# Kernel tuning notes

Hardware: AMD Instinct MI355X
Metric: run time of the kernel (lower is better)

The kernel has to match this reference:

```python
import jax, jax.numpy as jnp
import numpy as np

N = 50000   # nodes
E = 800000  # edges (avg degree 16)
D = 96      # feature dim for all layers


def setup_inputs() -> dict:
    key = jax.random.key(0)
    ks = jax.random.split(key, 8)
    x = jax.random.normal(ks[0], (N, D), dtype=jnp.float32)
    edge_index = jax.random.randint(ks[1], (2, E), 0, N, dtype=jnp.int32)
    edge_weight = jax.random.uniform(ks[2], (E,), dtype=jnp.float32)
    batch = jnp.zeros((N,), dtype=jnp.int32)  # unused by forward, kept for signature fidelity
    s = 1.0 / np.sqrt(D)
    W1 = jax.random.normal(ks[3], (D, D), dtype=jnp.float32) * s
    b1 = jnp.zeros((D,), dtype=jnp.float32)
    W2 = jax.random.normal(ks[4], (D, D), dtype=jnp.float32) * s
    b2 = jnp.zeros((D,), dtype=jnp.float32)
    return {"x": x, "edge_index": edge_index, "edge_weight": edge_weight,
            "batch": batch, "W1": W1, "b1": b1, "W2": W2, "b2": b2}


def gcn_conv(x, row, col, ew, W, b):
    """PyG GCNConv: add self-loops (weight 1), symmetric normalization,
    linear transform then weighted scatter-add aggregation at target (col)."""
    n = x.shape[0]
    h = x @ W  # [N, D_out]
    # degree includes self-loop weight 1.0
    deg = jax.ops.segment_sum(ew, col, num_segments=n) + 1.0
    dinv = jnp.where(deg > 0, jax.lax.rsqrt(deg), 0.0)
    norm = dinv[row] * ew * dinv[col]                      # [E]
    agg = jax.ops.segment_sum(h[row] * norm[:, None], col, num_segments=n)
    agg = agg + h * (dinv * dinv)[:, None]                 # self-loop messages
    return agg + b


def reference(x, edge_index, edge_weight, batch, W1, b1, W2, b2):
    row, col = edge_index[0], edge_index[1]
    # layer 1: conv -> relu (dropout p=0.0 is a no-op)
    h = jax.nn.relu(gcn_conv(x, row, col, edge_weight, W1, b1))
    # layer 2
    h = jax.nn.relu(gcn_conv(h, row, col, edge_weight, W2, b2))
    return h
```

## Files before the change

kernel.cpp:

```cpp
#include <hip/hip_runtime.h>
#include <hip/hip_fp16.h>

#define DIM 96
#define DIM4 (DIM/4)

typedef _Float16 f16x8 __attribute__((ext_vector_type(8)));
typedef float    f32x4 __attribute__((ext_vector_type(4)));

#define WSCALE 4194304.0f


#define PREP_BLOCKS 256

__global__ __launch_bounds__(256) void prep_kernel(unsigned long long* __restrict__ pdeg,
                                                   const float* __restrict__ W1,
                                                   const float* __restrict__ W2,
                                                   _Float16* __restrict__ Bt1,
                                                   _Float16* __restrict__ Bt2, int n) {
    for (int i = blockIdx.x * 256 + threadIdx.x; i < n; i += PREP_BLOCKS * 256)
        pdeg[i] = 0ULL;
    int i = blockIdx.x * 256 + threadIdx.x;
    if (i < DIM * DIM) {
        int c = i / DIM, k = i - c * DIM;
        Bt1[i] = (_Float16)W1[k * DIM + c];
        Bt2[i] = (_Float16)W2[k * DIM + c];
    }
}


__global__ void edge_pack_kernel(const int* __restrict__ col, const float* __restrict__ ew,
                                 unsigned long long* __restrict__ pdeg,
                                 int* __restrict__ rank, int e) {
    int i = blockIdx.x * blockDim.x + threadIdx.x;
    if (i < e) {
        unsigned q = (unsigned)(ew[i] * WSCALE + 0.5f);
        unsigned long long old =
            atomicAdd(&pdeg[col[i]], (1ULL << 32) | (unsigned long long)q);
        rank[i] = (int)(old >> 32);
    }
}


#define SCAN_BLK 256
#define SCAN_ELEMS 1024

__global__ __launch_bounds__(SCAN_BLK) void dinv_scanA_kernel(const unsigned long long* __restrict__ pdeg,
                                                              float* __restrict__ dinv,
                                                              int* __restrict__ cnt,
                                                              int* __restrict__ bsum, int n) {
    __shared__ int sdata[SCAN_BLK];
    int base = blockIdx.x * SCAN_ELEMS;
    int s = 0;
#pragma unroll
    for (int j = 0; j < 4; ++j) {
        int i = base + j * SCAN_BLK + (int)threadIdx.x;
        if (i < n) {
            unsigned long long p = pdeg[i];
            int c = (int)(p >> 32);
            cnt[i] = c;
            s += c;
            float deg = 1.0f + (float)(p & 0xffffffffULL) * (1.0f / WSCALE);
            dinv[i] = rsqrtf(deg);
        }
    }
    sdata[threadIdx.x] = s;
    __syncthreads();
    for (int off = SCAN_BLK / 2; off > 0; off >>= 1) {
        if (threadIdx.x < (unsigned)off) sdata[threadIdx.x] += sdata[threadIdx.x + off];
        __syncthreads();
    }
    if (threadIdx.x == 0) bsum[blockIdx.x] = sdata[0];
}

__global__ __launch_bounds__(1024) void scan_phaseB(int* __restrict__ bsum,
                                                    int* __restrict__ rowptr, int nb, int n) {
    __shared__ int sdata[1024];
    int v = (threadIdx.x < (unsigned)nb) ? bsum[threadIdx.x] : 0;
    sdata[threadIdx.x] = v;
    __syncthreads();
    for (int off = 1; off < 1024; off <<= 1) {
        int t = (threadIdx.x >= (unsigned)off) ? sdata[threadIdx.x - off] : 0;
        __syncthreads();
        sdata[threadIdx.x] += t;
        __syncthreads();
    }
    if (threadIdx.x < (unsigned)nb) bsum[threadIdx.x] = sdata[threadIdx.x] - v;
    if (threadIdx.x == (unsigned)(nb - 1)) rowptr[n] = sdata[threadIdx.x];
}

__global__ __launch_bounds__(SCAN_BLK) void scan_phaseC(const int* __restrict__ cnt,
                                                        const int* __restrict__ bsum,
                                                        int* __restrict__ rowptr, int n) {
    __shared__ int sdata[SCAN_BLK];
    int base = blockIdx.x * SCAN_ELEMS + (int)threadIdx.x * 4;
    int v[4];
#pragma unroll
    for (int j = 0; j < 4; ++j) v[j] = (base + j < n) ? cnt[base + j] : 0;
    int tsum = v[0] + v[1] + v[2] + v[3];
    sdata[threadIdx.x] = tsum;
    __syncthreads();
    for (int off = 1; off < SCAN_BLK; off <<= 1) {
        int t = (threadIdx.x >= (unsigned)off) ? sdata[threadIdx.x - off] : 0;
        __syncthreads();
        sdata[threadIdx.x] += t;
        __syncthreads();
    }
    int excl = bsum[blockIdx.x] + sdata[threadIdx.x] - tsum;
#pragma unroll
    for (int j = 0; j < 4; ++j) {
        if (base + j < n) rowptr[base + j] = excl;
        excl += v[j];
    }
}


__global__ void fill_kernel(const int* __restrict__ row, const int* __restrict__ col,
                            const float* __restrict__ ew, const float* __restrict__ dinv,
                            const int* __restrict__ rowptr, const int* __restrict__ rank,
                            int2* __restrict__ spack, int e) {
    int i = blockIdx.x * blockDim.x + threadIdx.x;
    if (i < e) {
        int c = col[i];
        int r = row[i];
        int p = rowptr[c] + rank[i];
        spack[p] = make_int2(r, __float_as_int(ew[i] * dinv[r]));
    }
}


template<bool A_IS_F32>
__global__ __launch_bounds__(256) void gemm_mfma_kernel(const void* __restrict__ Av,
                                                        const _Float16* __restrict__ Bt,
                                                        _Float16* __restrict__ H, int n) {
    int wave = threadIdx.x >> 6;
    int lane = threadIdx.x & 63;
    int r0 = blockIdx.x * 64 + wave * 16;
    if (r0 >= n) return;

    int lrow = lane & 15;
    int lk   = (lane >> 4) << 3;
    int arow = r0 + lrow;
    if (arow > n - 1) arow = n - 1;

    const _Float16* Ah = (const _Float16*)Av;
    const float*    Af = (const float*)Av;

    f32x4 acc[6] = {};

#pragma unroll
    for (int ks = 0; ks < 3; ++ks) {
        int k0 = ks * 32 + lk;
        f16x8 a;
        if (A_IS_F32) {
            const float* ap = Af + (size_t)arow * DIM + k0;
            float4 x0 = *(const float4*)ap;
            float4 x1 = *(const float4*)(ap + 4);
            a[0] = (_Float16)x0.x; a[1] = (_Float16)x0.y;
            a[2] = (_Float16)x0.z; a[3] = (_Float16)x0.w;
            a[4] = (_Float16)x1.x; a[5] = (_Float16)x1.y;
            a[6] = (_Float16)x1.z; a[7] = (_Float16)x1.w;
        } else {
            a = *(const f16x8*)(Ah + (size_t)arow * DIM + k0);
        }
#pragma unroll
        for (int ct = 0; ct < 6; ++ct) {
            f16x8 b = *(const f16x8*)(Bt + (size_t)(ct * 16 + lrow) * DIM + k0);
            acc[ct] = __builtin_amdgcn_mfma_f32_16x16x32_f16(a, b, acc[ct], 0, 0, 0);
        }
    }

    int crow = r0 + ((lane >> 4) << 2);
    int ccol = lane & 15;
#pragma unroll
    for (int ct = 0; ct < 6; ++ct) {
#pragma unroll
        for (int j = 0; j < 4; ++j) {
            int rr = crow + j;
            if (rr < n) H[(size_t)rr * DIM + ct * 16 + ccol] = (_Float16)acc[ct][j];
        }
    }
}


#define NPB 8

__device__ __forceinline__ float4 half4_to_float4(uint2 hv) {
    __half2 h01 = *(const __half2*)&hv.x;
    __half2 h23 = *(const __half2*)&hv.y;
    float2 f01 = __half22float2(h01);
    float2 f23 = __half22float2(h23);
    return make_float4(f01.x, f01.y, f23.x, f23.y);
}

template<bool OUT_F32>
__global__ __launch_bounds__(192) void gather_kernel(const int* __restrict__ rowptr,
                                                     const int2* __restrict__ spack,
                                                     const float* __restrict__ dinv,
                                                     const __half* __restrict__ H,
                                                     const float* __restrict__ bias,
                                                     float* __restrict__ outf,
                                                     __half* __restrict__ outh, int n) {
    int ln = threadIdx.x / 24;
    int q  = threadIdx.x - ln * 24;
    int node = blockIdx.x * NPB + ln;
    if (node >= n) return;

    int beg = rowptr[node];
    int end = rowptr[node + 1];
    float di = dinv[node];

    const uint2* Hq = (const uint2*)H;

    float4 acc = make_float4(0.f, 0.f, 0.f, 0.f);
    int p = beg;
    for (; p + 3 < end; p += 4) {
        int2 e0 = spack[p];
        int2 e1 = spack[p + 1];
        int2 e2 = spack[p + 2];
        int2 e3 = spack[p + 3];
        uint2 v0 = Hq[e0.x * 24 + q];
        uint2 v1 = Hq[e1.x * 24 + q];
        uint2 v2 = Hq[e2.x * 24 + q];
        uint2 v3 = Hq[e3.x * 24 + q];
        float w0 = __int_as_float(e0.y);
        float w1 = __int_as_float(e1.y);
        float w2 = __int_as_float(e2.y);
        float w3 = __int_as_float(e3.y);
        float4 h0 = half4_to_float4(v0);
        float4 h1 = half4_to_float4(v1);
        float4 h2 = half4_to_float4(v2);
        float4 h3 = half4_to_float4(v3);
        acc.x = fmaf(w0, h0.x, acc.x); acc.y = fmaf(w0, h0.y, acc.y);
        acc.z = fmaf(w0, h0.z, acc.z); acc.w = fmaf(w0, h0.w, acc.w);
        acc.x = fmaf(w1, h1.x, acc.x); acc.y = fmaf(w1, h1.y, acc.y);
        acc.z = fmaf(w1, h1.z, acc.z); acc.w = fmaf(w1, h1.w, acc.w);
        acc.x = fmaf(w2, h2.x, acc.x); acc.y = fmaf(w2, h2.y, acc.y);
        acc.z = fmaf(w2, h2.z, acc.z); acc.w = fmaf(w2, h2.w, acc.w);
        acc.x = fmaf(w3, h3.x, acc.x); acc.y = fmaf(w3, h3.y, acc.y);
        acc.z = fmaf(w3, h3.z, acc.z); acc.w = fmaf(w3, h3.w, acc.w);
    }
    for (; p < end; ++p) {
        int2 e0 = spack[p];
        float w0 = __int_as_float(e0.y);
        float4 h0 = half4_to_float4(Hq[e0.x * 24 + q]);
        acc.x = fmaf(w0, h0.x, acc.x); acc.y = fmaf(w0, h0.y, acc.y);
        acc.z = fmaf(w0, h0.z, acc.z); acc.w = fmaf(w0, h0.w, acc.w);
    }

    float s = di * di;
    float4 hc = half4_to_float4(Hq[node * 24 + q]);
    float4 b  = ((const float4*)bias)[q];

    float4 o;
    o.x = fmaxf(fmaf(hc.x, s, fmaf(acc.x, di, 0.f)) + b.x, 0.0f);
    o.y = fmaxf(fmaf(hc.y, s, fmaf(acc.y, di, 0.f)) + b.y, 0.0f);
    o.z = fmaxf(fmaf(hc.z, s, fmaf(acc.z, di, 0.f)) + b.z, 0.0f);
    o.w = fmaxf(fmaf(hc.w, s, fmaf(acc.w, di, 0.f)) + b.w, 0.0f);

    if (OUT_F32) {
        ((float4*)(outf + (size_t)node * DIM))[q] = o;
    } else {
        __half2 lo = __float22half2_rn(make_float2(o.x, o.y));
        __half2 hi = __float22half2_rn(make_float2(o.z, o.w));
        uint2 u;
        u.x = *(const unsigned*)&lo;
        u.y = *(const unsigned*)&hi;
        ((uint2*)(outh + (size_t)node * DIM))[q] = u;
    }
}


extern "C" void kernel_launch(void* const* d_in, const int* in_sizes, int n_in,
                              void* d_out, int out_size, void* d_ws, size_t ws_size,
                              hipStream_t stream) {
    const float* x   = (const float*)d_in[0];
    const int*   ei  = (const int*)d_in[1];
    const float* ew  = (const float*)d_in[2];
    const float* W1  = (const float*)d_in[4];
    const float* b1  = (const float*)d_in[5];
    const float* W2  = (const float*)d_in[6];
    const float* b2  = (const float*)d_in[7];

    const int N = in_sizes[0] / DIM;
    const int E = in_sizes[1] / 2;
    const int* row = ei;
    const int* col = ei + E;

    const int NB = (N + SCAN_ELEMS - 1) / SCAN_ELEMS;

    char* ws = (char*)d_ws;
    size_t off = 0;
    auto alloc = [&](size_t bytes) { void* p = ws + off; off = (off + bytes + 255) & ~(size_t)255; return p; };
    unsigned long long* pdeg = (unsigned long long*)alloc((size_t)N * 8);
    float* dinv   = (float*)alloc((size_t)N * 4);
    int*   cnt    = (int*)  alloc((size_t)N * 4);
    int*   rowptr = (int*)  alloc((size_t)(N + 1) * 4);
    int*   bsum   = (int*)  alloc((size_t)NB * 4);
    int*   rank   = (int*)  alloc((size_t)E * 4);
    int2*  spack  = (int2*) alloc((size_t)E * 8);
    _Float16* A   = (_Float16*)alloc((size_t)N * DIM * 2);
    _Float16* y1h = (_Float16*)alloc((size_t)N * DIM * 2);
    _Float16* Bt1 = (_Float16*)alloc((size_t)DIM * DIM * 2);
    _Float16* Bt2 = (_Float16*)alloc((size_t)DIM * DIM * 2);
    float* out    = (float*)d_out;

    dim3 blk(256);
    int gE  = (E + 255) / 256;
    int gMM = (N + 63) / 64;
    int gG  = (N + NPB - 1) / NPB;

    prep_kernel<<<PREP_BLOCKS, blk, 0, stream>>>(pdeg, W1, W2, Bt1, Bt2, N);
    edge_pack_kernel<<<gE, blk, 0, stream>>>(col, ew, pdeg, rank, E);
    dinv_scanA_kernel<<<NB, SCAN_BLK, 0, stream>>>(pdeg, dinv, cnt, bsum, N);
    scan_phaseB<<<1, 1024, 0, stream>>>(bsum, rowptr, NB, N);
    scan_phaseC<<<NB, SCAN_BLK, 0, stream>>>(cnt, bsum, rowptr, N);
    fill_kernel<<<gE, blk, 0, stream>>>(row, col, ew, dinv, rowptr, rank, spack, E);

    gemm_mfma_kernel<true><<<gMM, blk, 0, stream>>>(x, Bt1, A, N);
    gather_kernel<false><<<gG, 192, 0, stream>>>(rowptr, spack, dinv, (const __half*)A, b1,
                                                 nullptr, (__half*)y1h, N);

    gemm_mfma_kernel<false><<<gMM, blk, 0, stream>>>(y1h, Bt2, A, N);
    gather_kernel<true><<<gG, 192, 0, stream>>>(rowptr, spack, dinv, (const __half*)A, b2,
                                                out, nullptr, N);
}
```

Baseline: 157.4 us.

## Privatize degree atomics into 8 copies and fuse edge packing with first GEMM

Degree/count atomics are spread over eight private copies chosen by edge-block index, so fewer edges contend on each counter. Per-copy offsets are carried through the scan into a base table that the fill kernel uses. The edge-pack pass is also merged with the layer-1 GEMM into one launch by splitting the grid, so the atomic-bound and MFMA-bound work can overlap. The cost is eight times more zeroing and degree reads, plus an extra per-node offset table; the 16-bit offsets assume per-node degree below 65536.

```diff
diff --git a/kernel.cpp b/kernel.cpp
--- a/kernel.cpp
+++ b/kernel.cpp
@@ -8,16 +8,18 @@
 typedef float    f32x4 __attribute__((ext_vector_type(4)));
 
 #define WSCALE 4194304.0f
-
-
-#define PREP_BLOCKS 256
+#define NCOPY 8
+
+
+#define PREP_BLOCKS 512
 
 __global__ __launch_bounds__(256) void prep_kernel(unsigned long long* __restrict__ pdeg,
                                                    const float* __restrict__ W1,
                                                    const float* __restrict__ W2,
                                                    _Float16* __restrict__ Bt1,
                                                    _Float16* __restrict__ Bt2, int n) {
-    for (int i = blockIdx.x * 256 + threadIdx.x; i < n; i += PREP_BLOCKS * 256)
+    int total = n * NCOPY;
+    for (int i = blockIdx.x * 256 + threadIdx.x; i < total; i += PREP_BLOCKS * 256)
         pdeg[i] = 0ULL;
     int i = blockIdx.x * 256 + threadIdx.x;
     if (i < DIM * DIM) {
@@ -28,15 +30,58 @@
 }
 
 
-__global__ void edge_pack_kernel(const int* __restrict__ col, const float* __restrict__ ew,
-                                 unsigned long long* __restrict__ pdeg,
-                                 int* __restrict__ rank, int e) {
-    int i = blockIdx.x * blockDim.x + threadIdx.x;
-    if (i < e) {
-        unsigned q = (unsigned)(ew[i] * WSCALE + 0.5f);
-        unsigned long long old =
-            atomicAdd(&pdeg[col[i]], (1ULL << 32) | (unsigned long long)q);
-        rank[i] = (int)(old >> 32);
+__global__ __launch_bounds__(256) void fused_ep_gemm_kernel(
+        const int* __restrict__ col, const float* __restrict__ ew,
+        unsigned long long* __restrict__ pdeg, int* __restrict__ rank, int e, int n,
+        const float* __restrict__ X, const _Float16* __restrict__ Bt,
+        _Float16* __restrict__ H, int gmm) {
+    if ((int)blockIdx.x < gmm) {
+        int wave = threadIdx.x >> 6;
+        int lane = threadIdx.x & 63;
+        int r0 = blockIdx.x * 64 + wave * 16;
+        if (r0 >= n) return;
+        int lrow = lane & 15;
+        int lk   = (lane >> 4) << 3;
+        int arow = r0 + lrow;
+        if (arow > n - 1) arow = n - 1;
+
+        f32x4 acc[6] = {};
+#pragma unroll
+        for (int ks = 0; ks < 3; ++ks) {
+            int k0 = ks * 32 + lk;
+            const float* ap = X + (size_t)arow * DIM + k0;
+            float4 x0 = *(const float4*)ap;
+            float4 x1 = *(const float4*)(ap + 4);
+            f16x8 a;
+            a[0] = (_Float16)x0.x; a[1] = (_Float16)x0.y;
+            a[2] = (_Float16)x0.z; a[3] = (_Float16)x0.w;
+            a[4] = (_Float16)x1.x; a[5] = (_Float16)x1.y;
+            a[6] = (_Float16)x1.z; a[7] = (_Float16)x1.w;
+#pragma unroll
+            for (int ct = 0; ct < 6; ++ct) {
+                f16x8 b = *(const f16x8*)(Bt + (size_t)(ct * 16 + lrow) * DIM + k0);
+                acc[ct] = __builtin_amdgcn_mfma_f32_16x16x32_f16(a, b, acc[ct], 0, 0, 0);
+            }
+        }
+        int crow = r0 + ((lane >> 4) << 2);
+        int ccol = lane & 15;
+#pragma unroll
+        for (int ct = 0; ct < 6; ++ct)
+#pragma unroll
+            for (int j = 0; j < 4; ++j) {
+                int rr = crow + j;
+                if (rr < n) H[(size_t)rr * DIM + ct * 16 + ccol] = (_Float16)acc[ct][j];
+            }
+    } else {
+        int ebi = (int)blockIdx.x - gmm;
+        int i = ebi * 256 + (int)threadIdx.x;
+        if (i < e) {
+            int k = ebi & (NCOPY - 1);
+            unsigned q = (unsigned)(ew[i] * WSCALE + 0.5f);
+            unsigned long long old =
+                atomicAdd(&pdeg[(size_t)k * n + col[i]], (1ULL << 32) | (unsigned long long)q);
+            rank[i] = (int)(old >> 32);
+        }
     }
 }
 
@@ -47,6 +92,7 @@
 __global__ __launch_bounds__(SCAN_BLK) void dinv_scanA_kernel(const unsigned long long* __restrict__ pdeg,
                                                               float* __restrict__ dinv,
                                                               int* __restrict__ cnt,
+                                                              uint4* __restrict__ copyoff,
                                                               int* __restrict__ bsum, int n) {
     __shared__ int sdata[SCAN_BLK];
     int base = blockIdx.x * SCAN_ELEMS;
@@ -55,11 +101,21 @@
     for (int j = 0; j < 4; ++j) {
         int i = base + j * SCAN_BLK + (int)threadIdx.x;
         if (i < n) {
-            unsigned long long p = pdeg[i];
-            int c = (int)(p >> 32);
-            cnt[i] = c;
-            s += c;
-            float deg = 1.0f + (float)(p & 0xffffffffULL) * (1.0f / WSCALE);
+            uint4 off;
+            unsigned short* po = (unsigned short*)&off;
+            int run = 0;
+            unsigned long long wsum = 0;
+#pragma unroll
+            for (int k = 0; k < NCOPY; ++k) {
+                unsigned long long p = pdeg[(size_t)k * n + i];
+                po[k] = (unsigned short)run;
+                run += (int)(p >> 32);
+                wsum += (p & 0xffffffffULL);
+            }
+            cnt[i] = run;
+            s += run;
+            copyoff[i] = off;
+            float deg = 1.0f + (float)wsum * (1.0f / WSCALE);
             dinv[i] = rsqrtf(deg);
         }
     }
@@ -90,7 +146,9 @@
 
 __global__ __launch_bounds__(SCAN_BLK) void scan_phaseC(const int* __restrict__ cnt,
                                                         const int* __restrict__ bsum,
-                                                        int* __restrict__ rowptr, int n) {
+                                                        const uint4* __restrict__ copyoff,
+                                                        int* __restrict__ rowptr,
+                                                        int* __restrict__ basetab, int n) {
     __shared__ int sdata[SCAN_BLK];
     int base = blockIdx.x * SCAN_ELEMS + (int)threadIdx.x * 4;
     int v[4];
@@ -108,7 +166,15 @@
     int excl = bsum[blockIdx.x] + sdata[threadIdx.x] - tsum;
 #pragma unroll
     for (int j = 0; j < 4; ++j) {
-        if (base + j < n) rowptr[base + j] = excl;
+        int i = base + j;
+        if (i < n) {
+            rowptr[i] = excl;
+            uint4 off = copyoff[i];
+            const unsigned short* po = (const unsigned short*)&off;
+#pragma unroll
+            for (int k = 0; k < NCOPY; ++k)
+                basetab[(size_t)i * NCOPY + k] = excl + (int)po[k];
+        }
         excl += v[j];
     }
 }
@@ -116,20 +182,20 @@
 
 __global__ void fill_kernel(const int* __restrict__ row, const int* __restrict__ col,
                             const float* __restrict__ ew, const float* __restrict__ dinv,
-                            const int* __restrict__ rowptr, const int* __restrict__ rank,
+                            const int* __restrict__ basetab, const int* __restrict__ rank,
                             int2* __restrict__ spack, int e) {
     int i = blockIdx.x * blockDim.x + threadIdx.x;
     if (i < e) {
+        int k = (int)(blockIdx.x & (NCOPY - 1));
         int c = col[i];
         int r = row[i];
-        int p = rowptr[c] + rank[i];
+        int p = basetab[(size_t)c * NCOPY + k] + rank[i];
         spack[p] = make_int2(r, __float_as_int(ew[i] * dinv[r]));
     }
 }
 
 
-template<bool A_IS_F32>
-__global__ __launch_bounds__(256) void gemm_mfma_kernel(const void* __restrict__ Av,
+__global__ __launch_bounds__(256) void gemm_mfma_kernel(const _Float16* __restrict__ Ah,
                                                         const _Float16* __restrict__ Bt,
                                                         _Float16* __restrict__ H, int n) {
     int wave = threadIdx.x >> 6;
@@ -142,43 +208,26 @@
     int arow = r0 + lrow;
     if (arow > n - 1) arow = n - 1;
 
-    const _Float16* Ah = (const _Float16*)Av;
-    const float*    Af = (const float*)Av;
-
     f32x4 acc[6] = {};
-
 #pragma unroll
     for (int ks = 0; ks < 3; ++ks) {
         int k0 = ks * 32 + lk;
-        f16x8 a;
-        if (A_IS_F32) {
-            const float* ap = Af + (size_t)arow * DIM + k0;
-            float4 x0 = *(const float4*)ap;
-            float4 x1 = *(const float4*)(ap + 4);
-            a[0] = (_Float16)x0.x; a[1] = (_Float16)x0.y;
-            a[2] = (_Float16)x0.z; a[3] = (_Float16)x0.w;
-            a[4] = (_Float16)x1.x; a[5] = (_Float16)x1.y;
-            a[6] = (_Float16)x1.z; a[7] = (_Float16)x1.w;
-        } else {
-            a = *(const f16x8*)(Ah + (size_t)arow * DIM + k0);
-        }
+        f16x8 a = *(const f16x8*)(Ah + (size_t)arow * DIM + k0);
 #pragma unroll
         for (int ct = 0; ct < 6; ++ct) {
             f16x8 b = *(const f16x8*)(Bt + (size_t)(ct * 16 + lrow) * DIM + k0);
             acc[ct] = __builtin_amdgcn_mfma_f32_16x16x32_f16(a, b, acc[ct], 0, 0, 0);
         }
     }
-
     int crow = r0 + ((lane >> 4) << 2);
     int ccol = lane & 15;
 #pragma unroll
-    for (int ct = 0; ct < 6; ++ct) {
+    for (int ct = 0; ct < 6; ++ct)
 #pragma unroll
         for (int j = 0; j < 4; ++j) {
             int rr = crow + j;
             if (rr < n) H[(size_t)rr * DIM + ct * 16 + ccol] = (_Float16)acc[ct][j];
         }
-    }
 }
 
 
@@ -252,10 +301,10 @@
     float4 b  = ((const float4*)bias)[q];
 
     float4 o;
-    o.x = fmaxf(fmaf(hc.x, s, fmaf(acc.x, di, 0.f)) + b.x, 0.0f);
-    o.y = fmaxf(fmaf(hc.y, s, fmaf(acc.y, di, 0.f)) + b.y, 0.0f);
-    o.z = fmaxf(fmaf(hc.z, s, fmaf(acc.z, di, 0.f)) + b.z, 0.0f);
-    o.w = fmaxf(fmaf(hc.w, s, fmaf(acc.w, di, 0.f)) + b.w, 0.0f);
+    o.x = fmaxf(fmaf(hc.x, s, acc.x * di) + b.x, 0.0f);
+    o.y = fmaxf(fmaf(hc.y, s, acc.y * di) + b.y, 0.0f);
+    o.z = fmaxf(fmaf(hc.z, s, acc.z * di) + b.z, 0.0f);
+    o.w = fmaxf(fmaf(hc.w, s, acc.w * di) + b.w, 0.0f);
 
     if (OUT_F32) {
         ((float4*)(outf + (size_t)node * DIM))[q] = o;
@@ -291,11 +340,13 @@
     char* ws = (char*)d_ws;
     size_t off = 0;
     auto alloc = [&](size_t bytes) { void* p = ws + off; off = (off + bytes + 255) & ~(size_t)255; return p; };
-    unsigned long long* pdeg = (unsigned long long*)alloc((size_t)N * 8);
+    unsigned long long* pdeg = (unsigned long long*)alloc((size_t)N * NCOPY * 8);
     float* dinv   = (float*)alloc((size_t)N * 4);
     int*   cnt    = (int*)  alloc((size_t)N * 4);
     int*   rowptr = (int*)  alloc((size_t)(N + 1) * 4);
     int*   bsum   = (int*)  alloc((size_t)NB * 4);
+    uint4* copyoff= (uint4*)alloc((size_t)N * 16);
+    int*   basetab= (int*)  alloc((size_t)N * NCOPY * 4);
     int*   rank   = (int*)  alloc((size_t)E * 4);
     int2*  spack  = (int2*) alloc((size_t)E * 8);
     _Float16* A   = (_Float16*)alloc((size_t)N * DIM * 2);
@@ -310,17 +361,17 @@
     int gG  = (N + NPB - 1) / NPB;
 
     prep_kernel<<<PREP_BLOCKS, blk, 0, stream>>>(pdeg, W1, W2, Bt1, Bt2, N);
-    edge_pack_kernel<<<gE, blk, 0, stream>>>(col, ew, pdeg, rank, E);
-    dinv_scanA_kernel<<<NB, SCAN_BLK, 0, stream>>>(pdeg, dinv, cnt, bsum, N);
+    fused_ep_gemm_kernel<<<gMM + gE, blk, 0, stream>>>(col, ew, pdeg, rank, E, N,
+                                                       x, Bt1, A, gMM);
+    dinv_scanA_kernel<<<NB, SCAN_BLK, 0, stream>>>(pdeg, dinv, cnt, copyoff, bsum, N);
     scan_phaseB<<<1, 1024, 0, stream>>>(bsum, rowptr, NB, N);
-    scan_phaseC<<<NB, SCAN_BLK, 0, stream>>>(cnt, bsum, rowptr, N);
-    fill_kernel<<<gE, blk, 0, stream>>>(row, col, ew, dinv, rowptr, rank, spack, E);
-
-    gemm_mfma_kernel<true><<<gMM, blk, 0, stream>>>(x, Bt1, A, N);
+    scan_phaseC<<<NB, SCAN_BLK, 0, stream>>>(cnt, bsum, copyoff, rowptr, basetab, N);
+    fill_kernel<<<gE, blk, 0, stream>>>(row, col, ew, dinv, basetab, rank, spack, E);
+
     gather_kernel<false><<<gG, 192, 0, stream>>>(rowptr, spack, dinv, (const __half*)A, b1,
                                                  nullptr, (__half*)y1h, N);
 
-    gemm_mfma_kernel<false><<<gMM, blk, 0, stream>>>(y1h, Bt2, A, N);
+    gemm_mfma_kernel<<<gMM, blk, 0, stream>>>(y1h, Bt2, A, N);
     gather_kernel<true><<<gG, 192, 0, stream>>>(rowptr, spack, dinv, (const __half*)A, b2,
                                                 out, nullptr, N);
 }
```

Result: slower. 160.9 us (+2.2%).
